# Kernel tuning notes

Hardware: AMD Instinct MI355X
Metric: run time of the kernel (lower is better)

Reference implementation:

```python
import jax, jax.numpy as jnp
import numpy as np

B, S, D = 2, 1024, 4096
H, KV, HD = 32, 8, 128
GROUP = H // KV


def qlinear(x, w_int8, w_scale, bias):
    """Int8 dynamic-activation-quant linear: per-row activation scale, per-out-channel weight scale."""
    K = x.shape[-1]
    xf = x.reshape(-1, K)
    sx = jnp.max(jnp.abs(xf), axis=1, keepdims=True) / 127.0  # [M,1]
    sx = jnp.where(sx == 0, jnp.float32(1.0), sx)
    xi = jax.lax.stop_gradient(jnp.clip(jnp.round(xf / sx), -127.0, 127.0)).astype(jnp.int8)
    y = jnp.matmul(xi.astype(jnp.int32), w_int8.T.astype(jnp.int32)).astype(jnp.float32)  # int32 accum
    y = y * sx * w_scale[None, :]
    if bias is not None:
        y = y + bias
    return y.reshape(x.shape[:-1] + (w_int8.shape[0],))


def rope(t, c, s):
    half = t.shape[-1] // 2
    rot = jnp.concatenate([-t[..., half:], t[..., :half]], axis=-1)
    return t * c + rot * s


def setup_inputs() -> dict:
    key = jax.random.key(0)
    ks = jax.random.split(key, 10)
    x = jax.random.normal(ks[0], (B, S, D), dtype=jnp.float32)
    # RoPE tables (full-head_dim rotate-half convention)
    inv = 1.0 / (10000.0 ** (jnp.arange(0, HD, 2, dtype=jnp.float32) / HD))
    ang = jnp.arange(S, dtype=jnp.float32)[:, None] * inv[None, :]  # [S, HD/2]
    cos = jnp.concatenate([jnp.cos(ang), jnp.cos(ang)], axis=-1)
    sin = jnp.concatenate([jnp.sin(ang), jnp.sin(ang)], axis=-1)
    d_kv = KV * HD
    wq = jax.random.randint(ks[1], (H * HD, D), -127, 128, dtype=jnp.int32).astype(jnp.int8)
    wk = jax.random.randint(ks[2], (d_kv, D), -127, 128, dtype=jnp.int32).astype(jnp.int8)
    wv = jax.random.randint(ks[3], (d_kv, D), -127, 128, dtype=jnp.int32).astype(jnp.int8)
    wo = jax.random.randint(ks[4], (D, H * HD), -127, 128, dtype=jnp.int32).astype(jnp.int8)
    sc_in = jnp.float32(1.0 / (127.0 * np.sqrt(D)))
    sc_o = jnp.float32(1.0 / (127.0 * np.sqrt(H * HD)))
    sq = jnp.full((H * HD,), sc_in, dtype=jnp.float32)
    sk = jnp.full((d_kv,), sc_in, dtype=jnp.float32)
    sv = jnp.full((d_kv,), sc_in, dtype=jnp.float32)
    so = jnp.full((D,), sc_o, dtype=jnp.float32)
    bq = 0.01 * jax.random.normal(ks[5], (H * HD,), dtype=jnp.float32)
    bk = 0.01 * jax.random.normal(ks[6], (d_kv,), dtype=jnp.float32)
    bv = 0.01 * jax.random.normal(ks[7], (d_kv,), dtype=jnp.float32)
    return {"x": x, "cos": cos, "sin": sin, "wq": wq, "sq": sq, "bq": bq,
            "wk": wk, "sk": sk, "bk": bk, "wv": wv, "sv": sv, "bv": bv,
            "wo": wo, "so": so}


def reference(x, cos, sin, wq, sq, bq, wk, sk, bk, wv, sv, bv, wo, so):
    b, seq, _ = x.shape
    q = qlinear(x, wq, sq, bq).reshape(b, seq, H, HD)
    k = qlinear(x, wk, sk, bk).reshape(b, seq, KV, HD)
    v = qlinear(x, wv, sv, bv).reshape(b, seq, KV, HD)
    c = cos[:seq][None, :, None, :]
    s = sin[:seq][None, :, None, :]
    q = rope(q, c, s)
    k = rope(k, c, s)
    # start_pos=0 prefill: cache write then slice-back is identity -> use k, v directly.
    # GQA broadcast: q_head_to_kv_head = h // group_size
    idx = jnp.arange(H) // GROUP
    kf = k[:, :, idx, :]  # [b, seq, H, HD]
    vf = v[:, :, idx, :]
    scores = jnp.einsum('bqhd,bkhd->bhqk', q, kf) / jnp.sqrt(jnp.float32(HD))
    causal = jnp.tril(jnp.ones((seq, seq), dtype=bool))
    scores = jnp.where(causal[None, None, :, :], scores, jnp.float32(-jnp.inf))
    probs = jax.nn.softmax(scores, axis=-1)
    out = jnp.einsum('bhqk,bkhd->bqhd', probs, vf).reshape(b, seq, H * HD)
    return qlinear(out, wo, so, None)
```

## Files before the change

kernel.cpp:

```cpp
#include <hip/hip_runtime.h>


#define B_   2
#define S_   1024
#define D_   4096
#define H_   32
#define KV_  8
#define HD_  128
#define NR   (B_ * S_)
#define NQKV (H_*HD_ + 2*KV_*HD_)

typedef __attribute__((ext_vector_type(8))) short  short8;
typedef __attribute__((ext_vector_type(4))) float  f32x4;
typedef __attribute__((ext_vector_type(4))) int    int4v;

static __device__ __forceinline__ unsigned short f2bf(float f) {
    unsigned u = __builtin_bit_cast(unsigned, f);
    u += 0x7fffu + ((u >> 16) & 1u);
    return (unsigned short)(u >> 16);
}

static __device__ __forceinline__ void async_cp16(const void* g, void* l) {
    __builtin_amdgcn_global_load_lds(
        (const __attribute__((address_space(1))) void*)g,
        (__attribute__((address_space(3))) void*)l, 16, 0, 0);
}

__global__ __launch_bounds__(256) void quantize_rows_k(
    const float* __restrict__ X, signed char* __restrict__ Xq,
    float* __restrict__ sx_out, int K)
{
    int row = blockIdx.x;
    const float* xr = X + (size_t)row * K;
    int t = threadIdx.x;
    float m = 0.f;
    for (int j = t; j < K; j += 256) m = fmaxf(m, fabsf(xr[j]));
    for (int off = 32; off > 0; off >>= 1) m = fmaxf(m, __shfl_down(m, off, 64));
    __shared__ float red[4];
    if ((t & 63) == 0) red[t >> 6] = m;
    __syncthreads();
    float mm = fmaxf(fmaxf(red[0], red[1]), fmaxf(red[2], red[3]));
    float sx = mm / 127.0f;
    if (sx == 0.f) sx = 1.f;
    if (t == 0) sx_out[row] = sx;
    for (int j = t; j < K; j += 256) {
        float v = rintf(xr[j] / sx);
        v = fminf(fmaxf(v, -127.f), 127.f);
        Xq[(size_t)row * K + j] = (signed char)v;
    }
}

__global__ __launch_bounds__(256) void convert_w_i8(
    const int* __restrict__ W, signed char* __restrict__ Wb, int n16)
{
    int i = blockIdx.x * 256 + threadIdx.x;
    if (i >= n16) return;
    const int4v* src = (const int4v*)(W + (size_t)i * 16);
    int4v a = src[0], b = src[1], c = src[2], d = src[3];
    int4v o;
    o[0] = (a[0]&0xff) | ((a[1]&0xff)<<8) | ((a[2]&0xff)<<16) | ((a[3]&0xff)<<24);
    o[1] = (b[0]&0xff) | ((b[1]&0xff)<<8) | ((b[2]&0xff)<<16) | ((b[3]&0xff)<<24);
    o[2] = (c[0]&0xff) | ((c[1]&0xff)<<8) | ((c[2]&0xff)<<16) | ((c[3]&0xff)<<24);
    o[3] = (d[0]&0xff) | ((d[1]&0xff)<<8) | ((d[2]&0xff)<<16) | ((d[3]&0xff)<<24);
    *(int4v*)(Wb + (size_t)i * 16) = o;
}

template<int MODE>
__global__ __launch_bounds__(256) void gemm_i8_k(
    const signed char* __restrict__ A, const signed char* __restrict__ Bm,
    float* __restrict__ C, const float* __restrict__ rs,
    const float* __restrict__ cs, int K, int lda, int ldb, int ldc)
{
    __shared__ __align__(16) signed char As[128 * 64];
    __shared__ __align__(16) signed char Bs[128 * 64];

    int t    = threadIdx.x;
    int m0   = blockIdx.y * 128;
    int n0   = blockIdx.x * 128;
    int lane = t & 63;
    int w    = t >> 6;
    int wm   = (w >> 1) * 64;
    int wn   = (w & 1) * 64;
    int l15  = lane & 15;
    int quad = lane >> 4;

    int4v acc[4][4];
    #pragma unroll
    for (int i = 0; i < 4; i++)
        #pragma unroll
        for (int j = 0; j < 4; j++) { int4v z = {0,0,0,0}; acc[i][j] = z; }

    int srow = t >> 2;
    int scol = (t & 3) * 16;
    signed char* lA0 = As + w * 1024;
    signed char* lA1 = As + 4096 + w * 1024;
    signed char* lB0 = Bs + w * 1024;
    signed char* lB1 = Bs + 4096 + w * 1024;

    for (int k0 = 0; k0 < K; k0 += 64) {
        const signed char* ga = A  + (size_t)(m0 + srow) * lda + k0 + scol;
        const signed char* gb = Bm + (size_t)(n0 + srow) * ldb + k0 + scol;
        async_cp16(ga, lA0);
        async_cp16(ga + (size_t)64 * lda, lA1);
        async_cp16(gb, lB0);
        async_cp16(gb + (size_t)64 * ldb, lB1);
        __syncthreads();

        int4v af[4], bf[4];
        #pragma unroll
        for (int i = 0; i < 4; i++) {
            af[i] = *(const int4v*)&As[(wm + i*16 + l15) * 64 + quad * 16];
            bf[i] = *(const int4v*)&Bs[(wn + i*16 + l15) * 64 + quad * 16];
        }
        #pragma unroll
        for (int i = 0; i < 4; i++)
            #pragma unroll
            for (int j = 0; j < 4; j++)
                acc[i][j] = __builtin_amdgcn_mfma_i32_16x16x64_i8(af[i], bf[j], acc[i][j], 0, 0, 0);
        __syncthreads();
    }

    #pragma unroll
    for (int i = 0; i < 4; i++) {
        #pragma unroll
        for (int j = 0; j < 4; j++) {
            #pragma unroll
            for (int r = 0; r < 4; r++) {
                int row = m0 + wm + i*16 + quad*4 + r;
                int col = n0 + wn + j*16 + l15;
                float v = (float)acc[i][j][r];
                if (MODE == 3) v *= rs[row] * cs[col];
                C[(size_t)row * ldc + col] = v;
            }
        }
    }
}

__global__ __launch_bounds__(256) void derope_k(
    const float* __restrict__ Y, const float* __restrict__ sx,
    const float* __restrict__ sq, const float* __restrict__ bq,
    const float* __restrict__ sk, const float* __restrict__ bk,
    const float* __restrict__ sv, const float* __restrict__ bv,
    const float* __restrict__ cosb, const float* __restrict__ sinb,
    unsigned short* __restrict__ Q, unsigned short* __restrict__ Kb,
    unsigned short* __restrict__ Vt)
{
    const float qs = 0.08838834764831845f;
    int r = blockIdx.x;
    int b = r >> 10;
    int s = r & (S_ - 1);
    float sxr = sx[r];
    const float* yr = Y + (size_t)r * NQKV;
    int t = threadIdx.x;

    for (int p = t; p < H_ * 64; p += 256) {
        int h = p >> 6, d = p & 63;
        int ca = h * HD_ + d;
        float a  = yr[ca]      * sxr * sq[ca]      + bq[ca];
        float b2 = yr[ca + 64] * sxr * sq[ca + 64] + bq[ca + 64];
        float c  = cosb[s * HD_ + d], sn = sinb[s * HD_ + d];
        size_t base = (((size_t)(b * H_ + h)) * S_ + s) * HD_;
        Q[base + d]      = f2bf((a * c - b2 * sn) * qs);
        Q[base + d + 64] = f2bf((b2 * c + a * sn) * qs);
    }
    for (int p = t; p < KV_ * 64; p += 256) {
        int kv = p >> 6, d = p & 63;
        int ci = kv * HD_ + d;
        int ca = H_ * HD_ + ci;
        float a  = yr[ca]      * sxr * sk[ci]      + bk[ci];
        float b2 = yr[ca + 64] * sxr * sk[ci + 64] + bk[ci + 64];
        float c  = cosb[s * HD_ + d], sn = sinb[s * HD_ + d];
        size_t base = (((size_t)(b * KV_ + kv)) * S_ + s) * HD_;
        Kb[base + d]      = f2bf(a * c - b2 * sn);
        Kb[base + d + 64] = f2bf(b2 * c + a * sn);
    }
    for (int p = t; p < KV_ * HD_; p += 256) {
        int kv = p >> 7, d = p & 127;
        int ci = kv * HD_ + d;
        int ca = H_ * HD_ + KV_ * HD_ + ci;
        float v = yr[ca] * sxr * sv[ci] + bv[ci];
        size_t idx = (((size_t)(b * KV_ + kv)) * HD_ + d) * S_ + s;
        Vt[idx] = f2bf(v);
    }
}

__global__ __launch_bounds__(256) void flash_attn_k(
    const unsigned short* __restrict__ Qg,
    const unsigned short* __restrict__ Kg,
    const unsigned short* __restrict__ Vg,
    float* __restrict__ O)
{
    __shared__ __align__(16) unsigned short Ks[128 * HD_];
    __shared__ __align__(16) unsigned short Vs[HD_ * 128];

    int pair = blockIdx.x;
    int qt   = 7 - blockIdx.y;
    int b    = pair >> 5;
    int kv   = (pair & 31) >> 2;

    const unsigned short* Qb = Qg + ((size_t)pair * S_ + qt * 128) * HD_;
    const unsigned short* Kb = Kg + ((size_t)(b * KV_ + kv)) * (S_ * HD_);
    const unsigned short* Vb = Vg + ((size_t)(b * KV_ + kv)) * (HD_ * S_);

    int t    = threadIdx.x;
    int lane = t & 63;
    int w    = t >> 6;
    int l15  = lane & 15;
    int quad = lane >> 4;

    short8 qf[2][4];
    #pragma unroll
    for (int i = 0; i < 2; i++)
        #pragma unroll
        for (int ks = 0; ks < 4; ks++)
            qf[i][ks] = *(const short8*)(Qb + (size_t)(w*32 + i*16 + l15) * HD_ + ks*32 + quad*8);

    f32x4 oacc[2][8];
    #pragma unroll
    for (int i = 0; i < 2; i++)
        #pragma unroll
        for (int n = 0; n < 8; n++) { f32x4 z = {0.f,0.f,0.f,0.f}; oacc[i][n] = z; }
    float mrow[2][4], lrow[2][4];
    #pragma unroll
    for (int i = 0; i < 2; i++)
        #pragma unroll
        for (int r = 0; r < 4; r++) { mrow[i][r] = -1e30f; lrow[i][r] = 0.f; }

    for (int j = 0; j <= qt; ++j) {
        int k0 = j * 128;
        {
            const unsigned short* ksrc = Kb + (size_t)k0 * HD_ + t * 8;
            char* kdst = (char*)Ks + w * 1024;
            #pragma unroll
            for (int it = 0; it < 8; ++it)
                async_cp16(ksrc + it * 2048, kdst + it * 4096);
            const unsigned short* vsrc = Vb + (size_t)(w*4 + quad) * S_ + k0 + l15 * 8;
            char* vdst = (char*)Vs + w * 1024;
            #pragma unroll
            for (int it = 0; it < 8; ++it)
                async_cp16(vsrc + (size_t)it * 16 * S_, vdst + it * 4096);
        }
        __syncthreads();

        f32x4 sacc[2][8];
        #pragma unroll
        for (int i = 0; i < 2; i++)
            #pragma unroll
            for (int n = 0; n < 8; n++) { f32x4 z = {0.f,0.f,0.f,0.f}; sacc[i][n] = z; }
        #pragma unroll
        for (int n = 0; n < 8; n++) {
            short8 kf[4];
            #pragma unroll
            for (int ks = 0; ks < 4; ks++)
                kf[ks] = *(const short8*)&Ks[(n*16 + l15) * HD_ + ks*32 + quad*8];
            #pragma unroll
            for (int i = 0; i < 2; i++)
                #pragma unroll
                for (int ks = 0; ks < 4; ks++)
                    sacc[i][n] = __builtin_amdgcn_mfma_f32_16x16x32_bf16(qf[i][ks], kf[ks], sacc[i][n], 0, 0, 0);
        }

        if (j == qt) {
            #pragma unroll
            for (int i = 0; i < 2; i++)
                #pragma unroll
                for (int n = 0; n < 8; n++)
                    #pragma unroll
                    for (int r = 0; r < 4; r++) {
                        int qrow = w*32 + i*16 + quad*4 + r;
                        int kcol = n*16 + l15;
                        if (kcol > qrow) sacc[i][n][r] = -1e30f;
                    }
        }

        #pragma unroll
        for (int i = 0; i < 2; i++)
            #pragma unroll
            for (int r = 0; r < 4; r++) {
                float mx = sacc[i][0][r];
                #pragma unroll
                for (int n = 1; n < 8; n++) mx = fmaxf(mx, sacc[i][n][r]);
                mx = fmaxf(mx, __shfl_xor(mx, 1, 64));
                mx = fmaxf(mx, __shfl_xor(mx, 2, 64));
                mx = fmaxf(mx, __shfl_xor(mx, 4, 64));
                mx = fmaxf(mx, __shfl_xor(mx, 8, 64));
                float mnew = fmaxf(mrow[i][r], mx);
                float alpha = __expf(mrow[i][r] - mnew);
                mrow[i][r] = mnew;
                float s = 0.f;
                #pragma unroll
                for (int n = 0; n < 8; n++) {
                    float e = __expf(sacc[i][n][r] - mnew);
                    sacc[i][n][r] = e;
                    s += e;
                }
                s += __shfl_xor(s, 1, 64);
                s += __shfl_xor(s, 2, 64);
                s += __shfl_xor(s, 4, 64);
                s += __shfl_xor(s, 8, 64);
                lrow[i][r] = lrow[i][r] * alpha + s;
                #pragma unroll
                for (int n = 0; n < 8; n++) oacc[i][n][r] *= alpha;
            }

        __syncthreads();

        unsigned short* Ps = Ks;
        #pragma unroll
        for (int i = 0; i < 2; i++)
            #pragma unroll
            for (int n = 0; n < 8; n++)
                #pragma unroll
                for (int r = 0; r < 4; r++)
                    Ps[(size_t)(w*32 + i*16 + quad*4 + r) * 128 + n*16 + l15] =
                        f2bf(sacc[i][n][r]);

        short8 pf[2][4];
        #pragma unroll
        for (int i = 0; i < 2; i++)
            #pragma unroll
            for (int ks = 0; ks < 4; ks++)
                pf[i][ks] = *(const short8*)&Ps[(w*32 + i*16 + l15) * 128 + ks*32 + quad*8];
        #pragma unroll
        for (int n = 0; n < 8; n++) {
            short8 vf[4];
            #pragma unroll
            for (int ks = 0; ks < 4; ks++)
                vf[ks] = *(const short8*)&Vs[(n*16 + l15) * 128 + ks*32 + quad*8];
            #pragma unroll
            for (int i = 0; i < 2; i++)
                #pragma unroll
                for (int ks = 0; ks < 4; ks++)
                    oacc[i][n] = __builtin_amdgcn_mfma_f32_16x16x32_bf16(pf[i][ks], vf[ks], oacc[i][n], 0, 0, 0);
        }
        __syncthreads();
    }

    float* Ob = O + ((size_t)(b * S_ + qt * 128)) * (H_*HD_) + (pair & 31) * HD_;
    #pragma unroll
    for (int i = 0; i < 2; i++)
        #pragma unroll
        for (int r = 0; r < 4; r++) {
            float inv = 1.0f / lrow[i][r];
            int row = w*32 + i*16 + quad*4 + r;
            #pragma unroll
            for (int n = 0; n < 8; n++)
                Ob[(size_t)row * (H_*HD_) + n*16 + l15] = oacc[i][n][r] * inv;
        }
}

extern "C" void kernel_launch(void* const* d_in, const int* in_sizes, int n_in,
                              void* d_out, int out_size, void* d_ws, size_t ws_size,
                              hipStream_t stream)
{
    (void)in_sizes; (void)n_in; (void)out_size; (void)ws_size;
    const float* x    = (const float*)d_in[0];
    const float* cosb = (const float*)d_in[1];
    const float* sinb = (const float*)d_in[2];
    const int*   wq   = (const int*)d_in[3];
    const float* sq   = (const float*)d_in[4];
    const float* bq   = (const float*)d_in[5];
    const int*   wk   = (const int*)d_in[6];
    const float* sk   = (const float*)d_in[7];
    const float* bk   = (const float*)d_in[8];
    const int*   wv   = (const int*)d_in[9];
    const float* sv   = (const float*)d_in[10];
    const float* bv   = (const float*)d_in[11];
    const int*   wo   = (const int*)d_in[12];
    const float* so   = (const float*)d_in[13];
    float* out = (float*)d_out;
    char*  ws  = (char*)d_ws;

    signed char*    Xi   = (signed char*)(ws + 0);
    float*          Y    = (float*)(ws + 8388608ull);
    signed char*    Wqkv = (signed char*)(ws + 58720256ull);
    signed char*    Oi   = (signed char*)(ws + 58720256ull);
    signed char*    Wo   = (signed char*)(ws + 83886080ull);
    unsigned short* Q    = (unsigned short*)(ws + 100663296ull);
    unsigned short* Kb   = (unsigned short*)(ws + 117440512ull);
    unsigned short* Vt   = (unsigned short*)(ws + 121634816ull);
    float*          O    = (float*)(ws + 125829120ull);
    float*          sx   = (float*)(ws + 159383552ull);
    float*          sxo  = (float*)(ws + 159391744ull);

    quantize_rows_k<<<dim3(NR), dim3(256), 0, stream>>>(x, Xi, sx, D_);

    convert_w_i8<<<dim3(4096), dim3(256), 0, stream>>>(wq, Wqkv,            4096*256);
    convert_w_i8<<<dim3(1024), dim3(256), 0, stream>>>(wk, Wqkv + 16777216, 1024*256);
    convert_w_i8<<<dim3(1024), dim3(256), 0, stream>>>(wv, Wqkv + 20971520, 1024*256);
    convert_w_i8<<<dim3(4096), dim3(256), 0, stream>>>(wo, Wo,              4096*256);

    gemm_i8_k<0><<<dim3(48,16,1), dim3(256), 0, stream>>>(
        Xi, Wqkv, Y, nullptr, nullptr, D_, D_, D_, NQKV);

    derope_k<<<dim3(NR), dim3(256), 0, stream>>>(
        Y, sx, sq, bq, sk, bk, sv, bv, cosb, sinb, Q, Kb, Vt);

    flash_attn_k<<<dim3(64, 8), dim3(256), 0, stream>>>(Q, Kb, Vt, O);

    quantize_rows_k<<<dim3(NR), dim3(256), 0, stream>>>(O, Oi, sxo, H_*HD_);

    gemm_i8_k<3><<<dim3(32,16,1), dim3(256), 0, stream>>>(
        Oi, Wo, out, sxo, so, D_, D_, D_, D_);
}
```

Before: 488.0 us.

## Shrink attention tiles to 64, pad LDS, vectorize quantize, merge weight converts

The flash attention kernel now uses 64-row query and key tiles instead of 128, giving twice as many blocks and fewer registers per wave. K and V are staged through registers into LDS with padded row strides to avoid bank conflicts, replacing the async global-to-LDS copies. The row quantize kernel is vectorized with float4 loads and packed int8 stores, and the four weight-conversion launches are merged into one. The trade-off is more K/V reloads per query row, an extra barrier per tile, and the loss of the async copy path.

```diff
diff --git a/kernel.cpp b/kernel.cpp
--- a/kernel.cpp
+++ b/kernel.cpp
@@ -10,6 +10,9 @@
 #define NR   (B_ * S_)
 #define NQKV (H_*HD_ + 2*KV_*HD_)
 
+#define KSTR 132
+#define VSTR 68
+
 typedef __attribute__((ext_vector_type(8))) short  short8;
 typedef __attribute__((ext_vector_type(4))) float  f32x4;
 typedef __attribute__((ext_vector_type(4))) int    int4v;
@@ -28,13 +31,22 @@
 
 __global__ __launch_bounds__(256) void quantize_rows_k(
     const float* __restrict__ X, signed char* __restrict__ Xq,
-    float* __restrict__ sx_out, int K)
+    float* __restrict__ sx_out)
 {
     int row = blockIdx.x;
-    const float* xr = X + (size_t)row * K;
+    const f32x4* xr = (const f32x4*)(X + (size_t)row * 4096);
     int t = threadIdx.x;
+
+    f32x4 v[4];
+    #pragma unroll
+    for (int i = 0; i < 4; i++) v[i] = xr[t + i * 256];
+
     float m = 0.f;
-    for (int j = t; j < K; j += 256) m = fmaxf(m, fabsf(xr[j]));
+    #pragma unroll
+    for (int i = 0; i < 4; i++)
+        #pragma unroll
+        for (int j = 0; j < 4; j++) m = fmaxf(m, fabsf(v[i][j]));
+    #pragma unroll
     for (int off = 32; off > 0; off >>= 1) m = fmaxf(m, __shfl_down(m, off, 64));
     __shared__ float red[4];
     if ((t & 63) == 0) red[t >> 6] = m;
@@ -43,26 +55,41 @@
     float sx = mm / 127.0f;
     if (sx == 0.f) sx = 1.f;
     if (t == 0) sx_out[row] = sx;
-    for (int j = t; j < K; j += 256) {
-        float v = rintf(xr[j] / sx);
-        v = fminf(fmaxf(v, -127.f), 127.f);
-        Xq[(size_t)row * K + j] = (signed char)v;
-    }
-}
-
-__global__ __launch_bounds__(256) void convert_w_i8(
-    const int* __restrict__ W, signed char* __restrict__ Wb, int n16)
+
+    int* dst = (int*)(Xq + (size_t)row * 4096);
+    #pragma unroll
+    for (int i = 0; i < 4; i++) {
+        int o = 0;
+        #pragma unroll
+        for (int j = 0; j < 4; j++) {
+            float q = rintf(v[i][j] / sx);
+            q = fminf(fmaxf(q, -127.f), 127.f);
+            o |= (((int)q) & 0xff) << (j * 8);
+        }
+        dst[t + i * 256] = o;
+    }
+}
+
+__global__ __launch_bounds__(256) void convert_all_w(
+    const int* __restrict__ wq, const int* __restrict__ wk,
+    const int* __restrict__ wv, const int* __restrict__ wo,
+    signed char* __restrict__ Wqkv, signed char* __restrict__ Wo)
 {
     int i = blockIdx.x * 256 + threadIdx.x;
-    if (i >= n16) return;
-    const int4v* src = (const int4v*)(W + (size_t)i * 16);
-    int4v a = src[0], b = src[1], c = src[2], d = src[3];
+    const int* src;
+    signed char* dst;
+    if (i < 1048576)      { src = wq + (size_t)i * 16;              dst = Wqkv + (size_t)i * 16; }
+    else if (i < 1310720) { int j = i - 1048576; src = wk + (size_t)j * 16; dst = Wqkv + 16777216 + (size_t)j * 16; }
+    else if (i < 1572864) { int j = i - 1310720; src = wv + (size_t)j * 16; dst = Wqkv + 20971520 + (size_t)j * 16; }
+    else                  { int j = i - 1572864; src = wo + (size_t)j * 16; dst = Wo + (size_t)j * 16; }
+    const int4v* s4 = (const int4v*)src;
+    int4v a = s4[0], b = s4[1], c = s4[2], d = s4[3];
     int4v o;
     o[0] = (a[0]&0xff) | ((a[1]&0xff)<<8) | ((a[2]&0xff)<<16) | ((a[3]&0xff)<<24);
     o[1] = (b[0]&0xff) | ((b[1]&0xff)<<8) | ((b[2]&0xff)<<16) | ((b[3]&0xff)<<24);
     o[2] = (c[0]&0xff) | ((c[1]&0xff)<<8) | ((c[2]&0xff)<<16) | ((c[3]&0xff)<<24);
     o[3] = (d[0]&0xff) | ((d[1]&0xff)<<8) | ((d[2]&0xff)<<16) | ((d[3]&0xff)<<24);
-    *(int4v*)(Wb + (size_t)i * 16) = o;
+    *(int4v*)dst = o;
 }
 
 template<int MODE>
@@ -190,16 +217,16 @@
     const unsigned short* __restrict__ Vg,
     float* __restrict__ O)
 {
-    __shared__ __align__(16) unsigned short Ks[128 * HD_];
-    __shared__ __align__(16) unsigned short Vs[HD_ * 128];
+    __shared__ __align__(16) unsigned short Ks[64 * KSTR];
+    __shared__ __align__(16) unsigned short Vs[HD_ * VSTR];
 
     int pair = blockIdx.x;
-    int qt   = 7 - blockIdx.y;
+    int qt   = 15 - blockIdx.y;
     int b    = pair >> 5;
     int kv   = (pair & 31) >> 2;
 
-    const unsigned short* Qb = Qg + ((size_t)pair * S_ + qt * 128) * HD_;
-    const unsigned short* Kb = Kg + ((size_t)(b * KV_ + kv)) * (S_ * HD_);
+    const unsigned short* Qb = Qg + ((size_t)pair * S_ + qt * 64) * HD_;
+    const unsigned short* Kbp = Kg + ((size_t)(b * KV_ + kv)) * (S_ * HD_);
     const unsigned short* Vb = Vg + ((size_t)(b * KV_ + kv)) * (HD_ * S_);
 
     int t    = threadIdx.x;
@@ -208,145 +235,117 @@
     int l15  = lane & 15;
     int quad = lane >> 4;
 
-    short8 qf[2][4];
-    #pragma unroll
-    for (int i = 0; i < 2; i++)
-        #pragma unroll
-        for (int ks = 0; ks < 4; ks++)
-            qf[i][ks] = *(const short8*)(Qb + (size_t)(w*32 + i*16 + l15) * HD_ + ks*32 + quad*8);
-
-    f32x4 oacc[2][8];
-    #pragma unroll
-    for (int i = 0; i < 2; i++)
-        #pragma unroll
-        for (int n = 0; n < 8; n++) { f32x4 z = {0.f,0.f,0.f,0.f}; oacc[i][n] = z; }
-    float mrow[2][4], lrow[2][4];
-    #pragma unroll
-    for (int i = 0; i < 2; i++)
-        #pragma unroll
-        for (int r = 0; r < 4; r++) { mrow[i][r] = -1e30f; lrow[i][r] = 0.f; }
+    short8 qf[4];
+    #pragma unroll
+    for (int ks = 0; ks < 4; ks++)
+        qf[ks] = *(const short8*)(Qb + (size_t)(w*16 + l15) * HD_ + ks*32 + quad*8);
+
+    f32x4 oacc[8];
+    #pragma unroll
+    for (int n = 0; n < 8; n++) { f32x4 z = {0.f,0.f,0.f,0.f}; oacc[n] = z; }
+    float mrow[4], lrow[4];
+    #pragma unroll
+    for (int r = 0; r < 4; r++) { mrow[r] = -1e30f; lrow[r] = 0.f; }
+
+    int kr4 = t >> 4, kc = t & 15;
+    int vr4 = t >> 3, vc = t & 7;
 
     for (int j = 0; j <= qt; ++j) {
-        int k0 = j * 128;
-        {
-            const unsigned short* ksrc = Kb + (size_t)k0 * HD_ + t * 8;
-            char* kdst = (char*)Ks + w * 1024;
-            #pragma unroll
-            for (int it = 0; it < 8; ++it)
-                async_cp16(ksrc + it * 2048, kdst + it * 4096);
-            const unsigned short* vsrc = Vb + (size_t)(w*4 + quad) * S_ + k0 + l15 * 8;
-            char* vdst = (char*)Vs + w * 1024;
-            #pragma unroll
-            for (int it = 0; it < 8; ++it)
-                async_cp16(vsrc + (size_t)it * 16 * S_, vdst + it * 4096);
-        }
+        int k0 = j * 64;
         __syncthreads();
 
-        f32x4 sacc[2][8];
-        #pragma unroll
-        for (int i = 0; i < 2; i++)
-            #pragma unroll
-            for (int n = 0; n < 8; n++) { f32x4 z = {0.f,0.f,0.f,0.f}; sacc[i][n] = z; }
+        #pragma unroll
+        for (int p = 0; p < 4; ++p) {
+            int krow = p * 16 + kr4;
+            short8 kd = *(const short8*)(Kbp + (size_t)(k0 + krow) * HD_ + kc * 8);
+            *(short8*)&Ks[krow * KSTR + kc * 8] = kd;
+            int vrow = p * 32 + vr4;
+            short8 vd = *(const short8*)(Vb + (size_t)vrow * S_ + k0 + vc * 8);
+            *(short8*)&Vs[vrow * VSTR + vc * 8] = vd;
+        }
+        __syncthreads();
+
+        f32x4 sacc[4];
+        #pragma unroll
+        for (int n = 0; n < 4; n++) { f32x4 z = {0.f,0.f,0.f,0.f}; sacc[n] = z; }
+        #pragma unroll
+        for (int n = 0; n < 4; n++) {
+            #pragma unroll
+            for (int ks = 0; ks < 4; ks++) {
+                short8 kf = *(const short8*)&Ks[(n*16 + l15) * KSTR + ks*32 + quad*8];
+                sacc[n] = __builtin_amdgcn_mfma_f32_16x16x32_bf16(qf[ks], kf, sacc[n], 0, 0, 0);
+            }
+        }
+
+        if (j == qt) {
+            #pragma unroll
+            for (int n = 0; n < 4; n++)
+                #pragma unroll
+                for (int r = 0; r < 4; r++) {
+                    int qrow = w*16 + quad*4 + r;
+                    int kcol = n*16 + l15;
+                    if (kcol > qrow) sacc[n][r] = -1e30f;
+                }
+        }
+
+        #pragma unroll
+        for (int r = 0; r < 4; r++) {
+            float mx = fmaxf(fmaxf(sacc[0][r], sacc[1][r]), fmaxf(sacc[2][r], sacc[3][r]));
+            mx = fmaxf(mx, __shfl_xor(mx, 1, 64));
+            mx = fmaxf(mx, __shfl_xor(mx, 2, 64));
+            mx = fmaxf(mx, __shfl_xor(mx, 4, 64));
+            mx = fmaxf(mx, __shfl_xor(mx, 8, 64));
+            float mnew = fmaxf(mrow[r], mx);
+            float alpha = __expf(mrow[r] - mnew);
+            mrow[r] = mnew;
+            float s = 0.f;
+            #pragma unroll
+            for (int n = 0; n < 4; n++) {
+                float e = __expf(sacc[n][r] - mnew);
+                sacc[n][r] = e;
+                s += e;
+            }
+            s += __shfl_xor(s, 1, 64);
+            s += __shfl_xor(s, 2, 64);
+            s += __shfl_xor(s, 4, 64);
+            s += __shfl_xor(s, 8, 64);
+            lrow[r] = lrow[r] * alpha + s;
+            #pragma unroll
+            for (int n = 0; n < 8; n++) oacc[n][r] *= alpha;
+        }
+
+        __syncthreads();
+
+        unsigned short* Ps = Ks;
+        #pragma unroll
+        for (int n = 0; n < 4; n++)
+            #pragma unroll
+            for (int r = 0; r < 4; r++)
+                Ps[(w*16 + quad*4 + r) * KSTR + n*16 + l15] = f2bf(sacc[n][r]);
+
+        short8 pf[2];
+        #pragma unroll
+        for (int ks = 0; ks < 2; ks++)
+            pf[ks] = *(const short8*)&Ps[(w*16 + l15) * KSTR + ks*32 + quad*8];
         #pragma unroll
         for (int n = 0; n < 8; n++) {
-            short8 kf[4];
-            #pragma unroll
-            for (int ks = 0; ks < 4; ks++)
-                kf[ks] = *(const short8*)&Ks[(n*16 + l15) * HD_ + ks*32 + quad*8];
-            #pragma unroll
-            for (int i = 0; i < 2; i++)
-                #pragma unroll
-                for (int ks = 0; ks < 4; ks++)
-                    sacc[i][n] = __builtin_amdgcn_mfma_f32_16x16x32_bf16(qf[i][ks], kf[ks], sacc[i][n], 0, 0, 0);
-        }
-
-        if (j == qt) {
-            #pragma unroll
-            for (int i = 0; i < 2; i++)
-                #pragma unroll
-                for (int n = 0; n < 8; n++)
-                    #pragma unroll
-                    for (int r = 0; r < 4; r++) {
-                        int qrow = w*32 + i*16 + quad*4 + r;
-                        int kcol = n*16 + l15;
-                        if (kcol > qrow) sacc[i][n][r] = -1e30f;
-                    }
-        }
-
-        #pragma unroll
-        for (int i = 0; i < 2; i++)
-            #pragma unroll
-            for (int r = 0; r < 4; r++) {
-                float mx = sacc[i][0][r];
-                #pragma unroll
-                for (int n = 1; n < 8; n++) mx = fmaxf(mx, sacc[i][n][r]);
-                mx = fmaxf(mx, __shfl_xor(mx, 1, 64));
-                mx = fmaxf(mx, __shfl_xor(mx, 2, 64));
-                mx = fmaxf(mx, __shfl_xor(mx, 4, 64));
-                mx = fmaxf(mx, __shfl_xor(mx, 8, 64));
-                float mnew = fmaxf(mrow[i][r], mx);
-                float alpha = __expf(mrow[i][r] - mnew);
-                mrow[i][r] = mnew;
-                float s = 0.f;
-                #pragma unroll
-                for (int n = 0; n < 8; n++) {
-                    float e = __expf(sacc[i][n][r] - mnew);
-                    sacc[i][n][r] = e;
-                    s += e;
-                }
-                s += __shfl_xor(s, 1, 64);
-                s += __shfl_xor(s, 2, 64);
-                s += __shfl_xor(s, 4, 64);
-                s += __shfl_xor(s, 8, 64);
-                lrow[i][r] = lrow[i][r] * alpha + s;
-                #pragma unroll
-                for (int n = 0; n < 8; n++) oacc[i][n][r] *= alpha;
+            #pragma unroll
+            for (int ks = 0; ks < 2; ks++) {
+                short8 vf = *(const short8*)&Vs[(n*16 + l15) * VSTR + ks*32 + quad*8];
+                oacc[n] = __builtin_amdgcn_mfma_f32_16x16x32_bf16(pf[ks], vf, oacc[n], 0, 0, 0);
             }
-
-        __syncthreads();
-
-        unsigned short* Ps = Ks;
-        #pragma unroll
-        for (int i = 0; i < 2; i++)
-            #pragma unroll
-            for (int n = 0; n < 8; n++)
-                #pragma unroll
-                for (int r = 0; r < 4; r++)
-                    Ps[(size_t)(w*32 + i*16 + quad*4 + r) * 128 + n*16 + l15] =
-                        f2bf(sacc[i][n][r]);
-
-        short8 pf[2][4];
-        #pragma unroll
-        for (int i = 0; i < 2; i++)
-            #pragma unroll
-            for (int ks = 0; ks < 4; ks++)
-                pf[i][ks] = *(const short8*)&Ps[(w*32 + i*16 + l15) * 128 + ks*32 + quad*8];
-        #pragma unroll
-        for (int n = 0; n < 8; n++) {
-            short8 vf[4];
-            #pragma unroll
-            for (int ks = 0; ks < 4; ks++)
-                vf[ks] = *(const short8*)&Vs[(n*16 + l15) * 128 + ks*32 + quad*8];
-            #pragma unroll
-            for (int i = 0; i < 2; i++)
-                #pragma unroll
-                for (int ks = 0; ks < 4; ks++)
-                    oacc[i][n] = __builtin_amdgcn_mfma_f32_16x16x32_bf16(pf[i][ks], vf[ks], oacc[i][n], 0, 0, 0);
-        }
-        __syncthreads();
-    }
-
-    float* Ob = O + ((size_t)(b * S_ + qt * 128)) * (H_*HD_) + (pair & 31) * HD_;
-    #pragma unroll
-    for (int i = 0; i < 2; i++)
-        #pragma unroll
-        for (int r = 0; r < 4; r++) {
-            float inv = 1.0f / lrow[i][r];
-            int row = w*32 + i*16 + quad*4 + r;
-            #pragma unroll
-            for (int n = 0; n < 8; n++)
-                Ob[(size_t)row * (H_*HD_) + n*16 + l15] = oacc[i][n][r] * inv;
-        }
+        }
+    }
+
+    float* Ob = O + ((size_t)(b * S_ + qt * 64)) * (H_*HD_) + (pair & 31) * HD_;
+    #pragma unroll
+    for (int r = 0; r < 4; r++) {
+        float inv = 1.0f / lrow[r];
+        int row = w*16 + quad*4 + r;
+        #pragma unroll
+        for (int n = 0; n < 8; n++)
+            Ob[(size_t)row * (H_*HD_) + n*16 + l15] = oacc[n][r] * inv;
+    }
 }
 
 extern "C" void kernel_launch(void* const* d_in, const int* in_sizes, int n_in,
@@ -383,12 +382,9 @@
     float*          sx   = (float*)(ws + 159383552ull);
     float*          sxo  = (float*)(ws + 159391744ull);
 
-    quantize_rows_k<<<dim3(NR), dim3(256), 0, stream>>>(x, Xi, sx, D_);
-
-    convert_w_i8<<<dim3(4096), dim3(256), 0, stream>>>(wq, Wqkv,            4096*256);
-    convert_w_i8<<<dim3(1024), dim3(256), 0, stream>>>(wk, Wqkv + 16777216, 1024*256);
-    convert_w_i8<<<dim3(1024), dim3(256), 0, stream>>>(wv, Wqkv + 20971520, 1024*256);
-    convert_w_i8<<<dim3(4096), dim3(256), 0, stream>>>(wo, Wo,              4096*256);
+    quantize_rows_k<<<dim3(NR), dim3(256), 0, stream>>>(x, Xi, sx);
+
+    convert_all_w<<<dim3(10240), dim3(256), 0, stream>>>(wq, wk, wv, wo, Wqkv, Wo);
 
     gemm_i8_k<0><<<dim3(48,16,1), dim3(256), 0, stream>>>(
         Xi, Wqkv, Y, nullptr, nullptr, D_, D_, D_, NQKV);
@@ -396,9 +392,9 @@
     derope_k<<<dim3(NR), dim3(256), 0, stream>>>(
         Y, sx, sq, bq, sk, bk, sv, bv, cosb, sinb, Q, Kb, Vt);
 
-    flash_attn_k<<<dim3(64, 8), dim3(256), 0, stream>>>(Q, Kb, Vt, O);
-
-    quantize_rows_k<<<dim3(NR), dim3(256), 0, stream>>>(O, Oi, sxo, H_*HD_);
+    flash_attn_k<<<dim3(64, 16), dim3(256), 0, stream>>>(Q, Kb, Vt, O);
+
+    quantize_rows_k<<<dim3(NR), dim3(256), 0, stream>>>(O, Oi, sxo);
 
     gemm_i8_k<3><<<dim3(32,16,1), dim3(256), 0, stream>>>(
         Oi, Wo, out, sxo, so, D_, D_, D_, D_);
```

Measured after the change: 442.7 us. -9.3%, faster.
